# Kernel tuning notes

Measured on AMD Instinct MI355X. Metric: run time of the kernel, lower is better.

Reference implementation:

```python
import jax, jax.numpy as jnp
import numpy as np

TAU = 2.0
V_TH = 1.0


def setup_inputs() -> dict:
    key = jax.random.key(0)
    k_x, k_w1, k_w2 = jax.random.split(key, 3)
    T, B, N = 128, 64, 1024
    x = jax.random.normal(k_x, (T, B, N), dtype=jnp.float32)
    # nn.Linear(hidden, hidden, bias=False) weights: [out, in]
    scale = 1.0 / np.sqrt(N)
    w1 = jax.random.uniform(k_w1, (N, N), dtype=jnp.float32, minval=-scale, maxval=scale)
    w2 = jax.random.uniform(k_w2, (N, N), dtype=jnp.float32, minval=-scale, maxval=scale)
    return {"x": x, "w1": w1, "w2": w2}


def reference(x, w1, w2):
    # x: [T, B, N]; Linear with weight [out, in] -> x @ W^T
    T, B, N = x.shape
    h = jnp.einsum('tbn,mn->tbm', x, w1)  # fc1 applied per timestep

    def lif_step(v, h_t):
        # v: [B, N] membrane state; h_t: [B, N] input current
        hv = v + (h_t - v) / TAU
        s = (hv >= V_TH).astype(h_t.dtype)  # hard threshold spike
        v_next = hv * (1.0 - s)             # reset-to-zero on spike
        return v_next, s

    v0 = jnp.zeros((B, N), dtype=x.dtype)
    _, spikes = jax.lax.scan(lif_step, v0, h)  # spikes: [T, B, N]

    return jnp.einsum('tbn,mn->tbm', spikes, w2)  # fc2
```

## Files before the change

kernel.cpp:

```cpp
#include <hip/hip_runtime.h>
#include <hip/hip_bf16.h>

#define TT 128
#define BB 64
#define NN 1024

typedef __attribute__((ext_vector_type(4))) float f32x4;
typedef __attribute__((ext_vector_type(8))) short bf16x8;

#define FLAG_THR 2e-4
#define MAX_FLAG 16384

__device__ __forceinline__ unsigned short bf_hi_rne(float f, float& rem) {
    union { float f; unsigned int u; } c; c.f = f;
    const unsigned int r = c.u + 0x7fffu + ((c.u >> 16) & 1u);
    const unsigned short h = (unsigned short)(r >> 16);
    union { unsigned int u; float f; } b; b.u = ((unsigned int)h) << 16;
    rem = f - b.f;
    return h;
}

__global__ __launch_bounds__(256) void split_k(const float* __restrict__ X,
                                               unsigned short* __restrict__ XHi,
                                               unsigned short* __restrict__ XLo,
                                               const float* __restrict__ W,
                                               unsigned short* __restrict__ WHi,
                                               unsigned short* __restrict__ WLo,
                                               const float* __restrict__ W2,
                                               float* __restrict__ W2T,
                                               int* __restrict__ cnt) {
    __shared__ float tile[32][33];
    if (blockIdx.x == 0 && threadIdx.x == 0) *cnt = 0;

    if (blockIdx.x >= 9216) {
        const int tblk = blockIdx.x - 9216;
        const int tx  = threadIdx.x & 31;
        const int ty4 = (threadIdx.x >> 5) * 4;
        const int c0 = (tblk & 31) * 32;
        const int r0 = (tblk >> 5) * 32;
#pragma unroll
        for (int i = 0; i < 4; ++i)
            tile[ty4 + i][tx] = W2[(size_t)(r0 + ty4 + i) * NN + c0 + tx];
        __syncthreads();
#pragma unroll
        for (int i = 0; i < 4; ++i)
            W2T[(size_t)(c0 + ty4 + i) * NN + r0 + tx] = tile[tx][ty4 + i];
        return;
    }

    const bool isX = blockIdx.x < 8192;
    const float* A = isX ? X : W;
    unsigned short* Hi = isX ? XHi : WHi;
    unsigned short* Lo = isX ? XLo : WLo;
    const size_t blk = isX ? blockIdx.x : (blockIdx.x - 8192);
    const size_t f = (blk * 256 + threadIdx.x) * 4;
    const float4 v = *(const float4*)(A + f);
    float r, r2;
    ushort4 hi, lo;
    hi.x = bf_hi_rne(v.x, r); lo.x = bf_hi_rne(r, r2);
    hi.y = bf_hi_rne(v.y, r); lo.y = bf_hi_rne(r, r2);
    hi.z = bf_hi_rne(v.z, r); lo.z = bf_hi_rne(r, r2);
    hi.w = bf_hi_rne(v.w, r); lo.w = bf_hi_rne(r, r2);
    *(ushort4*)(Hi + f) = hi;
    *(ushort4*)(Lo + f) = lo;
}

#define STAGE(BI, KT)                                                         \
    {                                                                         \
        _Pragma("unroll")                                                     \
        for (int q = 0; q < 4; ++q) {                                         \
            const int slot = shalf + q * 64 + lane;                           \
            const int row  = slot >> 2;                                       \
            const int kc   = (slot & 3) ^ ((row >> 1) & 3);                   \
            const size_t grow = isA ? ((size_t)row * 64 + bm)                 \
                                    : ((size_t)bn * 128 + row);               \
            const unsigned short* gp =                                        \
                gsrc + grow * NN + (KT) * 32 + kc * 8;                        \
            __builtin_amdgcn_global_load_lds(                                 \
                (const __attribute__((address_space(1))) void*)gp,            \
                (__attribute__((address_space(3))) void*)(                    \
                    &ldsbuf[BI][buf][(wave & 1) * 2048 + q * 512]),           \
                16, 0, 0);                                                    \
        }                                                                     \
    }

#define COMPUTE(BI)                                                           \
    {                                                                         \
        const int c  = lane >> 4;                                             \
        const int rA = lane & 15;                                             \
        bf16x8 a0[4], a1[4], b0[2], b1[2];                                    \
        _Pragma("unroll")                                                     \
        for (int mf = 0; mf < 4; ++mf) {                                      \
            const int row = wm + mf * 16 + rA;                                \
            const int kc  = c ^ ((row >> 1) & 3);                             \
            a0[mf] = *(const bf16x8*)(&ldsbuf[BI][0][row * 32 + kc * 8]);     \
            a1[mf] = *(const bf16x8*)(&ldsbuf[BI][1][row * 32 + kc * 8]);     \
        }                                                                     \
        _Pragma("unroll")                                                     \
        for (int nf = 0; nf < 2; ++nf) {                                      \
            const int row = wn + nf * 16 + rA;                                \
            const int kc  = c ^ ((row >> 1) & 3);                             \
            b0[nf] = *(const bf16x8*)(&ldsbuf[BI][2][row * 32 + kc * 8]);     \
            b1[nf] = *(const bf16x8*)(&ldsbuf[BI][3][row * 32 + kc * 8]);     \
        }                                                                     \
        _Pragma("unroll")                                                     \
        for (int mf = 0; mf < 4; ++mf)                                        \
            _Pragma("unroll")                                                 \
            for (int nf = 0; nf < 2; ++nf) {                                  \
                acc[mf][nf] = __builtin_amdgcn_mfma_f32_16x16x32_bf16(        \
                    a0[mf], b0[nf], acc[mf][nf], 0, 0, 0);                    \
                acc[mf][nf] = __builtin_amdgcn_mfma_f32_16x16x32_bf16(        \
                    a0[mf], b1[nf], acc[mf][nf], 0, 0, 0);                    \
                acc[mf][nf] = __builtin_amdgcn_mfma_f32_16x16x32_bf16(        \
                    a1[mf], b0[nf], acc[mf][nf], 0, 0, 0);                    \
            }                                                                 \
    }

#define WAIT4 asm volatile("s_waitcnt vmcnt(4)" ::: "memory")
#define WAIT0 asm volatile("s_waitcnt vmcnt(0)" ::: "memory")
#define BARX   __builtin_amdgcn_s_barrier()
#define SCHED0 __builtin_amdgcn_sched_barrier(0)

__global__ __launch_bounds__(512, 4) void gemm1_lif_k(
    const unsigned short* __restrict__ A0g, const unsigned short* __restrict__ A1g,
    const unsigned short* __restrict__ B0g, const unsigned short* __restrict__ B1g,
    unsigned long long* __restrict__ M, int* __restrict__ counter,
    int* __restrict__ list) {
    __shared__ unsigned short ldsbuf[2][4][128 * 32];

    const int tid  = threadIdx.x;
    const int wave = tid >> 6;
    const int lane = tid & 63;
    const int bid = blockIdx.x;
    const int pos = bid >> 3;
    const int bm  = (bid & 7) * 8 + (pos >> 3);
    const int bn  = pos & 7;
    const int wm = (wave >> 2) * 64;
    const int wn = (wave & 3) * 32;

    f32x4 acc[4][2];
#pragma unroll
    for (int i = 0; i < 4; ++i)
#pragma unroll
        for (int j = 0; j < 2; ++j) acc[i][j] = (f32x4){0.f, 0.f, 0.f, 0.f};

    const int buf = wave >> 1;
    const unsigned short* gsrc =
        (buf == 0) ? A0g : (buf == 1) ? A1g : (buf == 2) ? B0g : B1g;
    const bool isA = (buf < 2);
    const int shalf = (wave & 1) * 256;

    STAGE(0, 0);
    STAGE(1, 1);

    for (int kt = 0; kt < 30; kt += 2) {
        WAIT4; BARX; SCHED0;
        COMPUTE(0);
        BARX;
        STAGE(0, kt + 2);
        WAIT4; BARX; SCHED0;
        COMPUTE(1);
        BARX;
        STAGE(1, kt + 3);
    }
    WAIT4; BARX; SCHED0;
    COMPUTE(0);
    BARX;
    WAIT0; BARX; SCHED0;
    COMPUTE(1);

    __syncthreads();
    float* htile = (float*)&ldsbuf[0][0][0];

    const int cr = lane >> 4, cc = lane & 15;
#pragma unroll
    for (int mf = 0; mf < 4; ++mf)
#pragma unroll
        for (int nf = 0; nf < 2; ++nf)
#pragma unroll
            for (int r = 0; r < 4; ++r) {
                const int t   = wm + mf * 16 + cr * 4 + r;
                const int col = wn + nf * 16 + cc;
                htile[t * 128 + (col ^ ((t & 7) << 2))] = acc[mf][nf][r];
            }
    __syncthreads();

    if (tid < 128) {
        const int col = tid;
        const int wv  = tid >> 6;
        double v = 0.0;
        bool flagged = false;
#pragma unroll 8
        for (int t = 0; t < TT; ++t) {
            const float hcur = htile[t * 128 + (col ^ ((t & 7) << 2))];
            const double hv = v + ((double)hcur - v) * 0.5;
            const bool s = (hv >= 1.0);
            flagged = flagged || (fabs(hv - 1.0) < FLAG_THR);
            const unsigned long long bmask = __ballot(s);
            if (lane == 0)
                M[(size_t)t * 1024 + bm * 16 + bn * 2 + wv] = bmask;
            v = s ? 0.0 : hv;
        }
        if (flagged) {
            const int idx = atomicAdd(counter, 1);
            if (idx < MAX_FLAG) list[idx] = bm * 1024 + bn * 128 + col;
        }
    }
}

__global__ __launch_bounds__(1024) void fixup_k(
    const float* __restrict__ X, const float* __restrict__ W1,
    unsigned long long* __restrict__ M, const int* __restrict__ counter,
    const int* __restrict__ list) {
    __shared__ double sv[128];
    __shared__ unsigned char sp[128];
    const int tid  = threadIdx.x;
    const int wave = tid >> 6;
    const int lane = tid & 63;
    int cnt = *counter; if (cnt > MAX_FLAG) cnt = MAX_FLAG;

    for (int ci = blockIdx.x; ci < cnt; ci += gridDim.x) {
        const int e = list[ci];
        const int b = e >> 10, n = e & 1023;

        double wk[16];
        {
            const float4* wr = (const float4*)(W1 + (size_t)n * NN);
#pragma unroll
            for (int j = 0; j < 4; ++j) {
                const float4 wv = wr[lane + 64 * j];
                wk[4 * j + 0] = (double)wv.x; wk[4 * j + 1] = (double)wv.y;
                wk[4 * j + 2] = (double)wv.z; wk[4 * j + 3] = (double)wv.w;
            }
        }
#pragma unroll
        for (int tt = 0; tt < 8; ++tt) {
            const int t = wave * 8 + tt;
            const float4* xr = (const float4*)(X + (size_t)(t * 64 + b) * NN);
            double s = 0.0;
#pragma unroll
            for (int j = 0; j < 4; ++j) {
                const float4 xv = xr[lane + 64 * j];
                s = fma((double)xv.x, wk[4 * j + 0], s);
                s = fma((double)xv.y, wk[4 * j + 1], s);
                s = fma((double)xv.z, wk[4 * j + 2], s);
                s = fma((double)xv.w, wk[4 * j + 3], s);
            }
#pragma unroll
            for (int off = 32; off > 0; off >>= 1) s += __shfl_xor(s, off);
            if (lane == 0) sv[t] = s;
        }
        __syncthreads();
        if (tid == 0) {
            double v = 0.0;
#pragma unroll
            for (int t = 0; t < TT; ++t) {
                const double hv = v + (sv[t] - v) * 0.5;
                const bool sf = (hv >= 1.0);
                sp[t] = sf;
                v = sf ? 0.0 : hv;
            }
        }
        __syncthreads();
        if (tid < 128) {
            const unsigned long long bit = 1ull << (e & 63);
            unsigned long long* mp = &M[(size_t)tid * 1024 + (e >> 6)];
            if (sp[tid]) atomicOr(mp, bit);
            else         atomicAnd(mp, ~bit);
        }
        __syncthreads();
    }
}

__global__ __launch_bounds__(256) void spmm2_k(const unsigned long long* __restrict__ M,
                                               const float* __restrict__ W2T,
                                               float* __restrict__ OUT) {
    __shared__ unsigned long long sm[16];
    const int r   = blockIdx.x;
    const int tid = threadIdx.x;
    if (tid < 16) sm[tid] = M[(size_t)r * 16 + tid];
    __syncthreads();

    double a0 = 0.0, a1 = 0.0, a2 = 0.0, a3 = 0.0;
    for (int w = 0; w < 16; ++w) {
        unsigned long long bits = sm[w];
        while (bits) {
            const int l = __builtin_ctzll(bits);
            bits &= bits - 1;
            const int n = w * 64 + l;
            const float4 wv = *(const float4*)&W2T[(size_t)n * NN + tid * 4];
            a0 += (double)wv.x; a1 += (double)wv.y;
            a2 += (double)wv.z; a3 += (double)wv.w;
        }
    }
    float4 o;
    o.x = (float)a0; o.y = (float)a1; o.z = (float)a2; o.w = (float)a3;
    *(float4*)&OUT[(size_t)r * NN + tid * 4] = o;
}

#define KT 32
#define SA 132
#define SB 68
__global__ __launch_bounds__(256) void gemm1_f64(const float* __restrict__ X,
                                                 const float* __restrict__ W1,
                                                 float* __restrict__ H) {
    __shared__ float As[KT][SA];
    __shared__ float Bs[KT][SB];
    const int tid = threadIdx.x;
    const int bm  = blockIdx.y;
    const int bn  = blockIdx.x;
    const int tm  = tid >> 4;
    const int tn  = tid & 15;
    const int lrow = tid >> 3;
    const int lk4  = (tid & 7) << 2;
    double acc[8][4];
#pragma unroll
    for (int i = 0; i < 8; ++i)
#pragma unroll
        for (int j = 0; j < 4; ++j) acc[i][j] = 0.0;
    for (int kt = 0; kt < NN; kt += KT) {
#pragma unroll
        for (int p = 0; p < 4; ++p) {
            const int m = lrow + p * 32;
            const float4 v = *(const float4*)&X[(size_t)(bm * 128 + m) * NN + kt + lk4];
            As[lk4 + 0][m] = v.x; As[lk4 + 1][m] = v.y;
            As[lk4 + 2][m] = v.z; As[lk4 + 3][m] = v.w;
        }
#pragma unroll
        for (int p = 0; p < 2; ++p) {
            const int n = lrow + p * 32;
            const float4 v = *(const float4*)&W1[(size_t)(bn * 64 + n) * NN + kt + lk4];
            Bs[lk4 + 0][n] = v.x; Bs[lk4 + 1][n] = v.y;
            Bs[lk4 + 2][n] = v.z; Bs[lk4 + 3][n] = v.w;
        }
        __syncthreads();
#pragma unroll
        for (int k = 0; k < KT; ++k) {
            float a[8], b[4];
            *(float4*)&a[0] = *(const float4*)&As[k][tm * 8];
            *(float4*)&a[4] = *(const float4*)&As[k][tm * 8 + 4];
            *(float4*)&b[0] = *(const float4*)&Bs[k][tn * 4];
#pragma unroll
            for (int i = 0; i < 8; ++i)
#pragma unroll
                for (int j = 0; j < 4; ++j)
                    acc[i][j] = fma((double)a[i], (double)b[j], acc[i][j]);
        }
        __syncthreads();
    }
#pragma unroll
    for (int i = 0; i < 8; ++i) {
        float4 v;
        v.x = (float)acc[i][0]; v.y = (float)acc[i][1];
        v.z = (float)acc[i][2]; v.w = (float)acc[i][3];
        *(float4*)&H[(size_t)(bm * 128 + tm * 8 + i) * NN + bn * 64 + tn * 4] = v;
    }
}

__global__ __launch_bounds__(256) void transp_k(const float* __restrict__ A,
                                                float* __restrict__ B) {
    __shared__ float tile[32][33];
    const int tx  = threadIdx.x & 31;
    const int ty4 = (threadIdx.x >> 5) * 4;
    const int c0 = blockIdx.x * 32;
    const int r0 = blockIdx.y * 32;
#pragma unroll
    for (int i = 0; i < 4; ++i)
        tile[ty4 + i][tx] = A[(size_t)(r0 + ty4 + i) * NN + c0 + tx];
    __syncthreads();
#pragma unroll
    for (int i = 0; i < 4; ++i)
        B[(size_t)(c0 + ty4 + i) * NN + r0 + tx] = tile[tx][ty4 + i];
}

__global__ __launch_bounds__(256) void lif_k(const float* __restrict__ H,
                                             unsigned long long* __restrict__ M,
                                             int* __restrict__ counter,
                                             int* __restrict__ list) {
    const int e    = blockIdx.x * 256 + threadIdx.x;
    const int lane = threadIdx.x & 63;
    const int word = e >> 6;
    double v = 0.0;
    bool flagged = false;

    float buf[8];
#pragma unroll
    for (int i = 0; i < 8; ++i) buf[i] = H[(size_t)i * 65536 + e];

#pragma unroll 8
    for (int t = 0; t < TT; ++t) {
        const float hcur = buf[t & 7];
        if (t + 8 < TT) buf[t & 7] = H[(size_t)(t + 8) * 65536 + e];
        const double hv = v + ((double)hcur - v) * 0.5;
        const bool s = (hv >= 1.0);
        flagged = flagged || (fabs(hv - 1.0) < FLAG_THR);
        const unsigned long long bmask = __ballot(s);
        if (lane == 0) M[(size_t)t * 1024 + word] = bmask;
        v = s ? 0.0 : hv;
    }
    if (flagged) {
        const int idx = atomicAdd(counter, 1);
        if (idx < MAX_FLAG) list[idx] = e;
    }
}

extern "C" void kernel_launch(void* const* d_in, const int* in_sizes, int n_in,
                              void* d_out, int out_size, void* d_ws, size_t ws_size,
                              hipStream_t stream) {
    const float* x  = (const float*)d_in[0];
    const float* w1 = (const float*)d_in[1];
    const float* w2 = (const float*)d_in[2];
    float* out = (float*)d_out;
    char* ws = (char*)d_ws;

    const size_t oH = 0, oW2T = 33554432, oM = 37748736;
    const size_t oB0 = 38797312, oB1 = 40894464;
    const size_t oA0 = 42991616, oA1 = 59768832;
    const size_t oCnt = 76546048, oList = 76546304;
    const size_t needFull = 76808448;

    float* h   = (float*)(ws + oH);
    float* w2t = (float*)(ws + oW2T);
    unsigned long long* masks = (unsigned long long*)(ws + oM);

    if (ws_size >= needFull) {
        unsigned short* B0s = (unsigned short*)(ws + oB0);
        unsigned short* B1s = (unsigned short*)(ws + oB1);
        unsigned short* A0g = (unsigned short*)(ws + oA0);
        unsigned short* A1g = (unsigned short*)(ws + oA1);
        int* cnt  = (int*)(ws + oCnt);
        int* list = (int*)(ws + oList);

        split_k<<<10240, 256, 0, stream>>>(x, A0g, A1g, w1, B0s, B1s, w2, w2t, cnt);
        gemm1_lif_k<<<512, 512, 0, stream>>>(A0g, A1g, B0s, B1s, masks, cnt, list);
        fixup_k<<<64, 1024, 0, stream>>>(x, w1, masks, cnt, list);
        spmm2_k<<<8192, 256, 0, stream>>>(masks, w2t, out);
    } else {
        int* cnt  = (int*)(ws + 38797312);
        int* list = (int*)(ws + 38797568);
        gemm1_f64<<<dim3(16, 64), 256, 0, stream>>>(x, w1, h);
        transp_k<<<dim3(32, 32), 256, 0, stream>>>(w2, w2t);
        hipMemsetAsync(cnt, 0, 4, stream);
        lif_k<<<256, 256, 0, stream>>>(h, masks, cnt, list);
        spmm2_k<<<8192, 256, 0, stream>>>(masks, w2t, out);
    }
}
```

Measured before the change: 98.71 us.

## Widen gemm1 block tile to 256 columns and share staging across waves

Doubles each gemm1_lif block's N tile from 128 to 256, so each wave computes a 64x64 output with 4x4 MFMA fragments. The grid shrinks from 512 to 256 blocks. Loads are now spread over all 8 waves at 6 loads per wave per stage, and the LIF scan runs on 256 threads. This raises reuse of the A tile and cuts redundant A loads, but it uses more LDS and registers and lowers occupancy to 2 blocks per CU, leaving fewer blocks to cover the 256 CUs.

```diff
diff --git a/kernel.cpp b/kernel.cpp
--- a/kernel.cpp
+++ b/kernel.cpp
@@ -65,48 +65,57 @@
     *(ushort4*)(Lo + f) = lo;
 }
 
-#define STAGE(BI, KT)                                                         \
+#define WAIT6 asm volatile("s_waitcnt vmcnt(6)" ::: "memory")
+#define WAIT0 asm volatile("s_waitcnt vmcnt(0)" ::: "memory")
+#define BARX   __builtin_amdgcn_s_barrier()
+#define SCHED0 __builtin_amdgcn_sched_barrier(0)
+
+#define STAGE(DST, KT)                                                        \
     {                                                                         \
         _Pragma("unroll")                                                     \
-        for (int q = 0; q < 4; ++q) {                                         \
-            const int slot = shalf + q * 64 + lane;                           \
-            const int row  = slot >> 2;                                       \
+        for (int q = 0; q < 6; ++q) {                                         \
+            const int slot0 = wave * 384 + q * 64;          \
+            const int slot  = slot0 + lane;                                   \
+            const int reg   = slot >> 9;               \
+            const unsigned short* gsrc =                                      \
+                (reg == 0) ? A0g : (reg == 1) ? A1g : (reg < 4) ? B0g : B1g;  \
+            const int ls   = (reg < 2) ? (slot & 511) : (slot & 1023);        \
+            const int row  = ls >> 2;                                         \
             const int kc   = (slot & 3) ^ ((row >> 1) & 3);                   \
-            const size_t grow = isA ? ((size_t)row * 64 + bm)                 \
-                                    : ((size_t)bn * 128 + row);               \
+            const size_t grow = (reg < 2) ? ((size_t)row * 64 + bm)           \
+                                          : ((size_t)bn * 256 + row);         \
             const unsigned short* gp =                                        \
                 gsrc + grow * NN + (KT) * 32 + kc * 8;                        \
             __builtin_amdgcn_global_load_lds(                                 \
                 (const __attribute__((address_space(1))) void*)gp,            \
-                (__attribute__((address_space(3))) void*)(                    \
-                    &ldsbuf[BI][buf][(wave & 1) * 2048 + q * 512]),           \
+                (__attribute__((address_space(3))) void*)((DST) + slot0 * 8), \
                 16, 0, 0);                                                    \
         }                                                                     \
     }
 
-#define COMPUTE(BI)                                                           \
+#define COMPUTE(SRC)                                                          \
     {                                                                         \
         const int c  = lane >> 4;                                             \
         const int rA = lane & 15;                                             \
-        bf16x8 a0[4], a1[4], b0[2], b1[2];                                    \
+        bf16x8 a0[4], a1[4], b0[4], b1[4];                                    \
         _Pragma("unroll")                                                     \
         for (int mf = 0; mf < 4; ++mf) {                                      \
             const int row = wm + mf * 16 + rA;                                \
             const int kc  = c ^ ((row >> 1) & 3);                             \
-            a0[mf] = *(const bf16x8*)(&ldsbuf[BI][0][row * 32 + kc * 8]);     \
-            a1[mf] = *(const bf16x8*)(&ldsbuf[BI][1][row * 32 + kc * 8]);     \
+            a0[mf] = *(const bf16x8*)((SRC) + row * 32 + kc * 8);             \
+            a1[mf] = *(const bf16x8*)((SRC) + 4096 + row * 32 + kc * 8);      \
         }                                                                     \
         _Pragma("unroll")                                                     \
-        for (int nf = 0; nf < 2; ++nf) {                                      \
+        for (int nf = 0; nf < 4; ++nf) {                                      \
             const int row = wn + nf * 16 + rA;                                \
             const int kc  = c ^ ((row >> 1) & 3);                             \
-            b0[nf] = *(const bf16x8*)(&ldsbuf[BI][2][row * 32 + kc * 8]);     \
-            b1[nf] = *(const bf16x8*)(&ldsbuf[BI][3][row * 32 + kc * 8]);     \
+            b0[nf] = *(const bf16x8*)((SRC) + 8192 + row * 32 + kc * 8);      \
+            b1[nf] = *(const bf16x8*)((SRC) + 16384 + row * 32 + kc * 8);     \
         }                                                                     \
         _Pragma("unroll")                                                     \
         for (int mf = 0; mf < 4; ++mf)                                        \
             _Pragma("unroll")                                                 \
-            for (int nf = 0; nf < 2; ++nf) {                                  \
+            for (int nf = 0; nf < 4; ++nf) {                                  \
                 acc[mf][nf] = __builtin_amdgcn_mfma_f32_16x16x32_bf16(        \
                     a0[mf], b0[nf], acc[mf][nf], 0, 0, 0);                    \
                 acc[mf][nf] = __builtin_amdgcn_mfma_f32_16x16x32_bf16(        \
@@ -116,94 +125,85 @@
             }                                                                 \
     }
 
-#define WAIT4 asm volatile("s_waitcnt vmcnt(4)" ::: "memory")
-#define WAIT0 asm volatile("s_waitcnt vmcnt(0)" ::: "memory")
-#define BARX   __builtin_amdgcn_s_barrier()
-#define SCHED0 __builtin_amdgcn_sched_barrier(0)
-
-__global__ __launch_bounds__(512, 4) void gemm1_lif_k(
+__global__ __launch_bounds__(512, 2) void gemm1_lif_k(
     const unsigned short* __restrict__ A0g, const unsigned short* __restrict__ A1g,
     const unsigned short* __restrict__ B0g, const unsigned short* __restrict__ B1g,
     unsigned long long* __restrict__ M, int* __restrict__ counter,
     int* __restrict__ list) {
-    __shared__ unsigned short ldsbuf[2][4][128 * 32];
+    __shared__ __align__(16) float smem[32768];
+    unsigned short* lds0 = (unsigned short*)smem;
+    unsigned short* lds1 = (unsigned short*)(smem + 12288);
+    float* htile = smem;
 
     const int tid  = threadIdx.x;
     const int wave = tid >> 6;
     const int lane = tid & 63;
     const int bid = blockIdx.x;
     const int pos = bid >> 3;
-    const int bm  = (bid & 7) * 8 + (pos >> 3);
-    const int bn  = pos & 7;
+    const int bm  = (bid & 7) * 8 + (pos >> 2);
+    const int bn  = pos & 3;
     const int wm = (wave >> 2) * 64;
-    const int wn = (wave & 3) * 32;
-
-    f32x4 acc[4][2];
+    const int wn = (wave & 3) * 64;
+
+    f32x4 acc[4][4];
 #pragma unroll
     for (int i = 0; i < 4; ++i)
 #pragma unroll
-        for (int j = 0; j < 2; ++j) acc[i][j] = (f32x4){0.f, 0.f, 0.f, 0.f};
-
-    const int buf = wave >> 1;
-    const unsigned short* gsrc =
-        (buf == 0) ? A0g : (buf == 1) ? A1g : (buf == 2) ? B0g : B1g;
-    const bool isA = (buf < 2);
-    const int shalf = (wave & 1) * 256;
-
-    STAGE(0, 0);
-    STAGE(1, 1);
+        for (int j = 0; j < 4; ++j) acc[i][j] = (f32x4){0.f, 0.f, 0.f, 0.f};
+
+    STAGE(lds0, 0);
+    STAGE(lds1, 1);
 
     for (int kt = 0; kt < 30; kt += 2) {
-        WAIT4; BARX; SCHED0;
-        COMPUTE(0);
+        WAIT6; BARX; SCHED0;
+        COMPUTE(lds0);
         BARX;
-        STAGE(0, kt + 2);
-        WAIT4; BARX; SCHED0;
-        COMPUTE(1);
+        STAGE(lds0, kt + 2);
+        WAIT6; BARX; SCHED0;
+        COMPUTE(lds1);
         BARX;
-        STAGE(1, kt + 3);
-    }
-    WAIT4; BARX; SCHED0;
-    COMPUTE(0);
+        STAGE(lds1, kt + 3);
+    }
+    WAIT6; BARX; SCHED0;
+    COMPUTE(lds0);
     BARX;
     WAIT0; BARX; SCHED0;
-    COMPUTE(1);
+    COMPUTE(lds1);
 
     __syncthreads();
-    float* htile = (float*)&ldsbuf[0][0][0];
 
     const int cr = lane >> 4, cc = lane & 15;
 #pragma unroll
     for (int mf = 0; mf < 4; ++mf)
 #pragma unroll
-        for (int nf = 0; nf < 2; ++nf)
+        for (int nf = 0; nf < 4; ++nf)
 #pragma unroll
             for (int r = 0; r < 4; ++r) {
                 const int t   = wm + mf * 16 + cr * 4 + r;
                 const int col = wn + nf * 16 + cc;
-                htile[t * 128 + (col ^ ((t & 7) << 2))] = acc[mf][nf][r];
+                htile[t * 256 + (col ^ ((t & 7) << 2))] = acc[mf][nf][r];
             }
     __syncthreads();
 
-    if (tid < 128) {
+    if (tid < 256) {
         const int col = tid;
         const int wv  = tid >> 6;
         double v = 0.0;
         bool flagged = false;
 #pragma unroll 8
         for (int t = 0; t < TT; ++t) {
-            const float hcur = htile[t * 128 + (col ^ ((t & 7) << 2))];
+            const float hcur = htile[t * 256 + (col ^ ((t & 7) << 2))];
             const double hv = v + ((double)hcur - v) * 0.5;
             const bool s = (hv >= 1.0);
             flagged = flagged || (fabs(hv - 1.0) < FLAG_THR);
             const unsigned long long bmask = __ballot(s);
             if (lane == 0)
-                M[(size_t)t * 1024 + bm * 16 + bn * 2 + wv] = bmask;
+                M[(size_t)t * 1024 + bm * 16 + bn * 4 + wv] = bmask;
             v = s ? 0.0 : hv;
         }
         if (flagged) {
             const int idx = atomicAdd(counter, 1);
-            if (idx < MAX_FLAG) list[idx] = bm * 1024 + bn * 128 + col;
+            if (idx < MAX_FLAG) list[idx] = bm * 1024 + bn * 256 + col;
         }
     }
 }
@@ -432,7 +432,7 @@
         int* list = (int*)(ws + oList);
 
         split_k<<<10240, 256, 0, stream>>>(x, A0g, A1g, w1, B0s, B1s, w2, w2t, cnt);
-        gemm1_lif_k<<<512, 512, 0, stream>>>(A0g, A1g, B0s, B1s, masks, cnt, list);
+        gemm1_lif_k<<<256, 512, 0, stream>>>(A0g, A1g, B0s, B1s, masks, cnt, list);
         fixup_k<<<64, 1024, 0, stream>>>(x, w1, masks, cnt, list);
         spmm2_k<<<8192, 256, 0, stream>>>(masks, w2t, out);
     } else {
```

Result: faster. 95.23 us (-3.5%).
